# Kernel tuning notes

Hardware: AMD Instinct MI355X
Metric: run time of the kernel (lower is better)

Reference implementation:

```python
import jax, jax.numpy as jnp
import numpy as np

N = 2_097_152   # batched ODE RHS evaluation points
T = 10_000      # forcing time-series length (days)
H = 16          # MLP hidden width


def _step(x):
    # smooth Heaviside used throughout EXP-Hydro
    return (jnp.tanh(5.0 * x) + 1.0) * 0.5


def _mlp(x, W1, b1, W2, b2, W3, b3):
    h = jnp.tanh(x @ W1 + b1)
    h = jnp.tanh(h @ W2 + b2)
    return (h @ W3 + b3)[..., 0]


def setup_inputs() -> dict:
    key = jax.random.key(0)
    ks = jax.random.split(key, 16)
    ts = jnp.arange(T, dtype=jnp.float32)
    inp = {
        "t": jax.random.uniform(ks[0], (N,), jnp.float32) * (T - 1),
        "S_snow": jax.random.uniform(ks[1], (N,), jnp.float32) * 50.0,
        "S_water": jax.random.uniform(ks[2], (N,), jnp.float32) * 1000.0,
        "ts": ts,
        "precp_series": jax.random.uniform(ks[3], (T,), jnp.float32) * 20.0,
        "temp_series": jax.random.normal(ks[4], (T,), jnp.float32) * 10.0,
        "lday_series": 0.3 + 0.4 * jax.random.uniform(ks[5], (T,), jnp.float32),
        "etW1": jax.random.normal(ks[6], (3, H), jnp.float32) * (1.0 / np.sqrt(3)),
        "etb1": jnp.zeros((H,), jnp.float32),
        "etW2": jax.random.normal(ks[7], (H, H), jnp.float32) * (1.0 / np.sqrt(H)),
        "etb2": jnp.zeros((H,), jnp.float32),
        "etW3": jax.random.normal(ks[8], (H, 1), jnp.float32) * (1.0 / np.sqrt(H)),
        "etb3": jnp.zeros((1,), jnp.float32),
        "qW1": jax.random.normal(ks[9], (2, H), jnp.float32) * (1.0 / np.sqrt(2)),
        "qb1": jnp.zeros((H,), jnp.float32),
        "qW2": jax.random.normal(ks[10], (H, H), jnp.float32) * (1.0 / np.sqrt(H)),
        "qb2": jnp.zeros((H,), jnp.float32),
        "qW3": jax.random.normal(ks[11], (H, 1), jnp.float32) * (1.0 / np.sqrt(H)),
        "qb3": jnp.zeros((1,), jnp.float32),
        "Df": jnp.float32(2.674),
        "Tmax": jnp.float32(0.176),
        "Tmin": jnp.float32(-2.093),
    }
    return inp


def reference(t, S_snow, S_water, ts, precp_series, temp_series, lday_series,
              etW1, etb1, etW2, etb2, etW3, etb3,
              qW1, qb1, qW2, qb2, qW3, qb3,
              Df, Tmax, Tmin):
    # linear interpolation of forcings at query times t  -> [N]
    precp = jnp.interp(t, ts, precp_series)
    temp = jnp.interp(t, ts, temp_series)
    lday = jnp.interp(t, ts, lday_series)

    ET = _mlp(jnp.stack([S_snow, S_water, temp], axis=-1),
              etW1, etb1, etW2, etb2, etW3, etb3)          # [N]
    Q = _mlp(jnp.stack([S_water, precp], axis=-1),
             qW1, qb1, qW2, qb2, qW3, qb3)                 # [N]

    # bucket physics (M / Ps / Pr with smooth step)
    melt = _step(temp - Tmax) * _step(S_snow) * jnp.minimum(S_snow, Df * (temp - Tmax))
    Ps = _step(Tmin - temp) * precp   # snowfall
    Pr = _step(temp - Tmin) * precp   # rainfall
    sw = _step(S_water)

    dS_1 = Ps - melt
    dS_2 = Pr + melt - sw * lday * jnp.exp(ET) - sw * jnp.exp(Q)
    return (dS_1, dS_2)
```

## Files before the change

### kernel.cpp

```cpp
#include <hip/hip_runtime.h>
#include <math.h>

#define BLOCK 256
#define PPT   2

typedef _Float16 half2v __attribute__((ext_vector_type(2)));
typedef _Float16 half4v __attribute__((ext_vector_type(4)));
typedef float    float4v __attribute__((ext_vector_type(4)));

__device__ __forceinline__ half2v cvt_pk_h2(float a, float b) {
    return __builtin_bit_cast(half2v, __builtin_amdgcn_cvt_pkrtz(a, b));
}

__device__ __forceinline__ half4v mk_h4(unsigned w0, unsigned w1) {
    uint2 u; u.x = w0; u.y = w1;
    return __builtin_bit_cast(half4v, u);
}

#define H4(x) {(_Float16)(x), (_Float16)(x), (_Float16)(x), (_Float16)(x)}

__device__ __forceinline__ half4v tanh_pk4(half4v x) {
    const half4v c5 = H4(-3.71625e-05f);
    const half4v c4 = H4( 1.09648e-03f);
    const half4v c3 = H4(-1.288264e-02f);
    const half4v c2 = H4( 7.941906e-02f);
    const half4v c1 = H4(-3.0042735e-01f);
    const half4v c0 = H4( 9.9607644e-01f);
    const half4v hi = H4( 3.0f);
    const half4v lo = H4(-3.0f);
    half4v t = __builtin_elementwise_min(__builtin_elementwise_max(x, lo), hi);
    half4v s = t * t;
#if __has_builtin(__builtin_elementwise_fma)
    half4v p = __builtin_elementwise_fma(c5, s, c4);
    p = __builtin_elementwise_fma(p, s, c3);
    p = __builtin_elementwise_fma(p, s, c2);
    p = __builtin_elementwise_fma(p, s, c1);
    p = __builtin_elementwise_fma(p, s, c0);
#else
    half4v p = c5 * s + c4;
    p = p * s + c3;
    p = p * s + c2;
    p = p * s + c1;
    p = p * s + c0;
#endif
    return t * p;
}

__device__ __forceinline__ half4v pk4_from_f32(float a, float b, float c, float d) {
    half2v lo = cvt_pk_h2(a, b);
    half2v hi = cvt_pk_h2(c, d);
    return __builtin_shufflevector(lo, hi, 0, 1, 2, 3);
}

__device__ __forceinline__ half4v act4(float4v d) {
    return tanh_pk4(pk4_from_f32(d[0], d[1], d[2], d[3]));
}

#if __has_builtin(__builtin_amdgcn_permlane16_swap) && __has_builtin(__builtin_amdgcn_permlane32_swap)
#define SWAP16X(XV_) ({ auto _r = __builtin_amdgcn_permlane16_swap((XV_), (XV_), false, false); \
                        (unsigned)(_r[0] ^ _r[1] ^ (XV_)); })
#define SWAP32X(XV_) ({ auto _r = __builtin_amdgcn_permlane32_swap((XV_), (XV_), false, false); \
                        (unsigned)(_r[0] ^ _r[1] ^ (XV_)); })
#else
#define SWAP16X(XV_) ((unsigned)__shfl((int)(XV_), lane ^ 16, 64))
#define SWAP32X(XV_) ((unsigned)__shfl((int)(XV_), lane ^ 32, 64))
#endif

__global__ __launch_bounds__(BLOCK) void pack_forcings_kernel(
    const float* __restrict__ precp_s, const float* __restrict__ temp_s,
    const float* __restrict__ lday_s, float4* __restrict__ F, int T)
{
    int i = blockIdx.x * BLOCK + threadIdx.x;
    if (i < T) F[i] = make_float4(precp_s[i], temp_s[i], lday_s[i], 0.0f);
}

#define MFMA16(A, B, C) __builtin_amdgcn_mfma_f32_16x16x16f16((A), (B), (C), 0, 0, 0)

__global__ __launch_bounds__(BLOCK, 4) void exphydro_mfma_kernel(
    const float* __restrict__ t, const float* __restrict__ S_snow,
    const float* __restrict__ S_water,
    const float4* __restrict__ F,
    const float* __restrict__ etW1, const float* __restrict__ etb1,
    const float* __restrict__ etW2, const float* __restrict__ etb2,
    const float* __restrict__ etW3, const float* __restrict__ etb3,
    const float* __restrict__ qW1, const float* __restrict__ qb1,
    const float* __restrict__ qW2, const float* __restrict__ qb2,
    const float* __restrict__ qW3, const float* __restrict__ qb3,
    const float* __restrict__ pDf, const float* __restrict__ pTmax,
    const float* __restrict__ pTmin,
    float* __restrict__ out, int N, int T)
{
    const int lane = threadIdx.x & 63;
    const int hi   = lane >> 4;
    const int m    = lane & 15;
    const int wave = threadIdx.x >> 6;
    const int base = blockIdx.x * (BLOCK * PPT) + wave * (64 * PPT);

    half4v A1et, A1q, A2et, A2q, A3et, A3q;
    float4v C2et, C2q, C3et, C3q;
    #pragma unroll
    for (int j = 0; j < 4; j++) {
        int k = 4 * hi + j;
        float w1e = (k < 3) ? etW1[k * 16 + m] : ((k == 3) ? etb1[m] : 0.0f);
        float w1q = (k < 2) ? qW1 [k * 16 + m] : ((k == 2) ? qb1 [m] : 0.0f);
        A1et[j] = (_Float16)w1e;
        A1q [j] = (_Float16)w1q;
        A2et[j] = (_Float16)etW2[k * 16 + m];
        A2q [j] = (_Float16)qW2 [k * 16 + m];
        A3et[j] = (_Float16)etW3[k];
        A3q [j] = (_Float16)qW3 [k];
        C2et[j] = etb2[4 * hi + j];
        C2q [j] = qb2 [4 * hi + j];
        C3et[j] = etb3[0];
        C3q [j] = qb3 [0];
    }

    const float Df   = pDf[0];
    const float Tmax = pTmax[0];
    const float Tmin = pTmin[0];
    const float tmaxf = (float)(T - 1);
    const int   imax  = T - 2;

#define LOAD_POINT(U, Pv, SSv, SWv, TPv, PRv, LDv, I01v, I23v)                 \
    const int Pv = base + (U) * 64 + lane;                                     \
    float SSv, SWv, TPv, PRv, LDv; unsigned I01v, I23v;                        \
    {                                                                          \
        int pc = (Pv < N) ? Pv : (N - 1);                                      \
        float tv = t[pc];                                                      \
        SSv = S_snow[pc];                                                      \
        SWv = S_water[pc];                                                     \
        float tc = fminf(fmaxf(tv, 0.0f), tmaxf);                              \
        int i0 = (int)tc;                                                      \
        i0 = (i0 > imax) ? imax : i0;                                          \
        float fr = tc - (float)i0;                                             \
        float4 f0 = F[i0];                                                     \
        float4 f1 = F[i0 + 1];                                                 \
        PRv = fmaf(fr, f1.x - f0.x, f0.x);                                     \
        TPv = fmaf(fr, f1.y - f0.y, f0.y);                                     \
        LDv = fmaf(fr, f1.z - f0.z, f0.z);                                     \
        I01v = __builtin_bit_cast(unsigned, cvt_pk_h2(SSv, SWv));              \
        I23v = __builtin_bit_cast(unsigned, cvt_pk_h2(TPv, PRv));              \
    }

    LOAD_POINT(0, p0, ss0, sw0, tp0, pr0, ld0, i01_0, i23_0)
    LOAD_POINT(1, p1, ss1, sw1, tp1, pr1, ld1, i01_1, i23_1)

    const float4v zero4 = {0.0f, 0.0f, 0.0f, 0.0f};

#define MLP_SET(I01v, I23v, E0, E1, E2, E3, Q0, Q1, Q2, Q3)                    \
    float E0, E1, E2, E3, Q0, Q1, Q2, Q3;                                      \
    {                                                                          \
                              \
        unsigned j01_0 = I01v;                                                 \
        unsigned j23_0 = I23v;                                                 \
        unsigned j01_1 = SWAP16X(I01v);                                        \
        unsigned j23_1 = SWAP16X(I23v);                                        \
        unsigned j01_2 = SWAP32X(I01v);                                        \
        unsigned j23_2 = SWAP32X(I23v);                                        \
        unsigned j01_3 = SWAP16X(j01_2);                                       \
        unsigned j23_3 = SWAP16X(j23_2);                                       \
                                          \
        float4v d1e0 = MFMA16(A1et, mk_h4(j01_0, 0x3C000000u | (j23_0 & 0xFFFFu)), zero4); \
        float4v d1q0 = MFMA16(A1q,  mk_h4((j01_0 >> 16) | (j23_0 & 0xFFFF0000u), 0x3C00u), zero4); \
        float4v d1e1 = MFMA16(A1et, mk_h4(j01_1, 0x3C000000u | (j23_1 & 0xFFFFu)), zero4); \
        float4v d1q1 = MFMA16(A1q,  mk_h4((j01_1 >> 16) | (j23_1 & 0xFFFF0000u), 0x3C00u), zero4); \
        float4v d1e2 = MFMA16(A1et, mk_h4(j01_2, 0x3C000000u | (j23_2 & 0xFFFFu)), zero4); \
        float4v d1q2 = MFMA16(A1q,  mk_h4((j01_2 >> 16) | (j23_2 & 0xFFFF0000u), 0x3C00u), zero4); \
        float4v d1e3 = MFMA16(A1et, mk_h4(j01_3, 0x3C000000u | (j23_3 & 0xFFFFu)), zero4); \
        float4v d1q3 = MFMA16(A1q,  mk_h4((j01_3 >> 16) | (j23_3 & 0xFFFF0000u), 0x3C00u), zero4); \
                                       \
        half4v b2e0 = act4(d1e0);  half4v b2q0 = act4(d1q0);                   \
        half4v b2e1 = act4(d1e1);  half4v b2q1 = act4(d1q1);                   \
        half4v b2e2 = act4(d1e2);  half4v b2q2 = act4(d1q2);                   \
        half4v b2e3 = act4(d1e3);  half4v b2q3 = act4(d1q3);                   \
                                                          \
        float4v d2e0 = MFMA16(A2et, b2e0, C2et);  float4v d2q0 = MFMA16(A2q, b2q0, C2q); \
        float4v d2e1 = MFMA16(A2et, b2e1, C2et);  float4v d2q1 = MFMA16(A2q, b2q1, C2q); \
        float4v d2e2 = MFMA16(A2et, b2e2, C2et);  float4v d2q2 = MFMA16(A2q, b2q2, C2q); \
        float4v d2e3 = MFMA16(A2et, b2e3, C2et);  float4v d2q3 = MFMA16(A2q, b2q3, C2q); \
                                                       \
        half4v b3e0 = act4(d2e0);  half4v b3q0 = act4(d2q0);                   \
        half4v b3e1 = act4(d2e1);  half4v b3q1 = act4(d2q1);                   \
        half4v b3e2 = act4(d2e2);  half4v b3q2 = act4(d2q2);                   \
        half4v b3e3 = act4(d2e3);  half4v b3q3 = act4(d2q3);                   \
                                                          \
        float4v d3e0 = MFMA16(A3et, b3e0, C3et);  float4v d3q0 = MFMA16(A3q, b3q0, C3q); \
        float4v d3e1 = MFMA16(A3et, b3e1, C3et);  float4v d3q1 = MFMA16(A3q, b3q1, C3q); \
        float4v d3e2 = MFMA16(A3et, b3e2, C3et);  float4v d3q2 = MFMA16(A3q, b3q2, C3q); \
        float4v d3e3 = MFMA16(A3et, b3e3, C3et);  float4v d3q3 = MFMA16(A3q, b3q3, C3q); \
        E0 = d3e0[0]; E1 = d3e1[0]; E2 = d3e2[0]; E3 = d3e3[0];                \
        Q0 = d3q0[0]; Q1 = d3q1[0]; Q2 = d3q2[0]; Q3 = d3q3[0];                \
    }

    MLP_SET(i01_0, i23_0, et00, et01, et02, et03, q00, q01, q02, q03)
    MLP_SET(i01_1, i23_1, et10, et11, et12, et13, q10, q11, q12, q13)

#define FINISH_POINT(Pv, SSv, SWv, TPv, PRv, LDv, E0, E1, E2, E3, Q0, Q1, Q2, Q3) \
    {                                                                          \
        float e01s = (lane & 16) ? E1 : E0;                                    \
        float e23s = (lane & 16) ? E3 : E2;                                    \
        float ET   = (lane & 32) ? e23s : e01s;                                \
        float q01s = (lane & 16) ? Q1 : Q0;                                    \
        float q23s = (lane & 16) ? Q3 : Q2;                                    \
        float Q    = (lane & 32) ? q23s : q01s;                                \
        float dT = TPv - Tmax;                                                 \
        half4v sargs = pk4_from_f32(5.0f * dT, 5.0f * SSv,                     \
                                    5.0f * (Tmin - TPv), 5.0f * SWv);          \
        half4v th = tanh_pk4(sargs);                                           \
        float stepA  = fmaf(0.5f, (float)th[0], 0.5f);                         \
        float stepSn = fmaf(0.5f, (float)th[1], 0.5f);                         \
        float stepPs = fmaf(0.5f, (float)th[2], 0.5f);                         \
        float sw01   = fmaf(0.5f, (float)th[3], 0.5f);                         \
        float melt = stepA * stepSn * fminf(SSv, Df * dT);                     \
        float Ps   = stepPs * PRv;                                             \
        float Pr   = (1.0f - stepPs) * PRv;                                    \
        float dS1 = Ps - melt;                                                 \
        float dS2 = Pr + melt - sw01 * (LDv * __expf(ET) + __expf(Q));         \
        if (Pv < N) {                                                          \
            out[Pv]     = dS1;                                                 \
            out[N + Pv] = dS2;                                                 \
        }                                                                      \
    }

    FINISH_POINT(p0, ss0, sw0, tp0, pr0, ld0, et00, et01, et02, et03, q00, q01, q02, q03)
    FINISH_POINT(p1, ss1, sw1, tp1, pr1, ld1, et10, et11, et12, et13, q10, q11, q12, q13)
}

extern "C" void kernel_launch(void* const* d_in, const int* in_sizes, int n_in,
                              void* d_out, int out_size, void* d_ws, size_t ws_size,
                              hipStream_t stream) {
    const float* t        = (const float*)d_in[0];
    const float* S_snow   = (const float*)d_in[1];
    const float* S_water  = (const float*)d_in[2];
    const float* precp_s  = (const float*)d_in[4];
    const float* temp_s   = (const float*)d_in[5];
    const float* lday_s   = (const float*)d_in[6];
    const float* etW1     = (const float*)d_in[7];
    const float* etb1     = (const float*)d_in[8];
    const float* etW2     = (const float*)d_in[9];
    const float* etb2     = (const float*)d_in[10];
    const float* etW3     = (const float*)d_in[11];
    const float* etb3     = (const float*)d_in[12];
    const float* qW1      = (const float*)d_in[13];
    const float* qb1      = (const float*)d_in[14];
    const float* qW2      = (const float*)d_in[15];
    const float* qb2      = (const float*)d_in[16];
    const float* qW3      = (const float*)d_in[17];
    const float* qb3      = (const float*)d_in[18];
    const float* pDf      = (const float*)d_in[19];
    const float* pTmax    = (const float*)d_in[20];
    const float* pTmin    = (const float*)d_in[21];

    int N = in_sizes[0];
    int T = in_sizes[3];
    float* out = (float*)d_out;
    float4* F = (float4*)d_ws;

    pack_forcings_kernel<<<(T + BLOCK - 1) / BLOCK, BLOCK, 0, stream>>>(
        precp_s, temp_s, lday_s, F, T);

    int per_block = BLOCK * PPT;
    exphydro_mfma_kernel<<<(N + per_block - 1) / per_block, BLOCK, 0, stream>>>(
        t, S_snow, S_water, F,
        etW1, etb1, etW2, etb2, etW3, etb3,
        qW1, qb1, qW2, qb2, qW3, qb3,
        pDf, pTmax, pTmin, out, N, T);
}
```

Baseline: 41.80 us.

## Process four points per thread with all loads hoisted and per-point MLP scoping

Raises points per thread from 2 to 4, issuing every gather and load up front and then running the MLP and finish step one point at a time in separate scopes to bound register lifetimes. It also swaps the packed order of precipitation and temperature so the MFMA operand assembly uses a shift and alignbit instead of masks and ORs. The aim is more memory-level parallelism and fewer packing instructions, at the cost of higher register pressure and fewer blocks in the grid.

```diff
diff --git a/kernel.cpp b/kernel.cpp
--- a/kernel.cpp
+++ b/kernel.cpp
@@ -2,7 +2,7 @@
 #include <math.h>
 
 #define BLOCK 256
-#define PPT   2
+#define PPT   4
 
 typedef _Float16 half2v __attribute__((ext_vector_type(2)));
 typedef _Float16 half4v __attribute__((ext_vector_type(4)));
@@ -139,18 +139,19 @@
         TPv = fmaf(fr, f1.y - f0.y, f0.y);                                     \
         LDv = fmaf(fr, f1.z - f0.z, f0.z);                                     \
         I01v = __builtin_bit_cast(unsigned, cvt_pk_h2(SSv, SWv));              \
-        I23v = __builtin_bit_cast(unsigned, cvt_pk_h2(TPv, PRv));              \
+        I23v = __builtin_bit_cast(unsigned, cvt_pk_h2(PRv, TPv));              \
     }
 
     LOAD_POINT(0, p0, ss0, sw0, tp0, pr0, ld0, i01_0, i23_0)
     LOAD_POINT(1, p1, ss1, sw1, tp1, pr1, ld1, i01_1, i23_1)
+    LOAD_POINT(2, p2, ss2, sw2, tp2, pr2, ld2, i01_2, i23_2)
+    LOAD_POINT(3, p3, ss3, sw3, tp3, pr3, ld3, i01_3, i23_3)
 
     const float4v zero4 = {0.0f, 0.0f, 0.0f, 0.0f};
 
 #define MLP_SET(I01v, I23v, E0, E1, E2, E3, Q0, Q1, Q2, Q3)                    \
     float E0, E1, E2, E3, Q0, Q1, Q2, Q3;                                      \
     {                                                                          \
-                              \
         unsigned j01_0 = I01v;                                                 \
         unsigned j23_0 = I23v;                                                 \
         unsigned j01_1 = SWAP16X(I01v);                                        \
@@ -159,31 +160,26 @@
         unsigned j23_2 = SWAP32X(I23v);                                        \
         unsigned j01_3 = SWAP16X(j01_2);                                       \
         unsigned j23_3 = SWAP16X(j23_2);                                       \
-                                          \
-        float4v d1e0 = MFMA16(A1et, mk_h4(j01_0, 0x3C000000u | (j23_0 & 0xFFFFu)), zero4); \
-        float4v d1q0 = MFMA16(A1q,  mk_h4((j01_0 >> 16) | (j23_0 & 0xFFFF0000u), 0x3C00u), zero4); \
-        float4v d1e1 = MFMA16(A1et, mk_h4(j01_1, 0x3C000000u | (j23_1 & 0xFFFFu)), zero4); \
-        float4v d1q1 = MFMA16(A1q,  mk_h4((j01_1 >> 16) | (j23_1 & 0xFFFF0000u), 0x3C00u), zero4); \
-        float4v d1e2 = MFMA16(A1et, mk_h4(j01_2, 0x3C000000u | (j23_2 & 0xFFFFu)), zero4); \
-        float4v d1q2 = MFMA16(A1q,  mk_h4((j01_2 >> 16) | (j23_2 & 0xFFFF0000u), 0x3C00u), zero4); \
-        float4v d1e3 = MFMA16(A1et, mk_h4(j01_3, 0x3C000000u | (j23_3 & 0xFFFFu)), zero4); \
-        float4v d1q3 = MFMA16(A1q,  mk_h4((j01_3 >> 16) | (j23_3 & 0xFFFF0000u), 0x3C00u), zero4); \
-                                       \
+        float4v d1e0 = MFMA16(A1et, mk_h4(j01_0, 0x3C000000u | (j23_0 >> 16)), zero4); \
+        float4v d1q0 = MFMA16(A1q,  mk_h4(__builtin_amdgcn_alignbit(j23_0, j01_0, 16), 0x3C00u), zero4); \
+        float4v d1e1 = MFMA16(A1et, mk_h4(j01_1, 0x3C000000u | (j23_1 >> 16)), zero4); \
+        float4v d1q1 = MFMA16(A1q,  mk_h4(__builtin_amdgcn_alignbit(j23_1, j01_1, 16), 0x3C00u), zero4); \
+        float4v d1e2 = MFMA16(A1et, mk_h4(j01_2, 0x3C000000u | (j23_2 >> 16)), zero4); \
+        float4v d1q2 = MFMA16(A1q,  mk_h4(__builtin_amdgcn_alignbit(j23_2, j01_2, 16), 0x3C00u), zero4); \
+        float4v d1e3 = MFMA16(A1et, mk_h4(j01_3, 0x3C000000u | (j23_3 >> 16)), zero4); \
+        float4v d1q3 = MFMA16(A1q,  mk_h4(__builtin_amdgcn_alignbit(j23_3, j01_3, 16), 0x3C00u), zero4); \
         half4v b2e0 = act4(d1e0);  half4v b2q0 = act4(d1q0);                   \
         half4v b2e1 = act4(d1e1);  half4v b2q1 = act4(d1q1);                   \
         half4v b2e2 = act4(d1e2);  half4v b2q2 = act4(d1q2);                   \
         half4v b2e3 = act4(d1e3);  half4v b2q3 = act4(d1q3);                   \
-                                                          \
         float4v d2e0 = MFMA16(A2et, b2e0, C2et);  float4v d2q0 = MFMA16(A2q, b2q0, C2q); \
         float4v d2e1 = MFMA16(A2et, b2e1, C2et);  float4v d2q1 = MFMA16(A2q, b2q1, C2q); \
         float4v d2e2 = MFMA16(A2et, b2e2, C2et);  float4v d2q2 = MFMA16(A2q, b2q2, C2q); \
         float4v d2e3 = MFMA16(A2et, b2e3, C2et);  float4v d2q3 = MFMA16(A2q, b2q3, C2q); \
-                                                       \
         half4v b3e0 = act4(d2e0);  half4v b3q0 = act4(d2q0);                   \
         half4v b3e1 = act4(d2e1);  half4v b3q1 = act4(d2q1);                   \
         half4v b3e2 = act4(d2e2);  half4v b3q2 = act4(d2q2);                   \
         half4v b3e3 = act4(d2e3);  half4v b3q3 = act4(d2q3);                   \
-                                                          \
         float4v d3e0 = MFMA16(A3et, b3e0, C3et);  float4v d3q0 = MFMA16(A3q, b3q0, C3q); \
         float4v d3e1 = MFMA16(A3et, b3e1, C3et);  float4v d3q1 = MFMA16(A3q, b3q1, C3q); \
         float4v d3e2 = MFMA16(A3et, b3e2, C3et);  float4v d3q2 = MFMA16(A3q, b3q2, C3q); \
@@ -191,9 +187,6 @@
         E0 = d3e0[0]; E1 = d3e1[0]; E2 = d3e2[0]; E3 = d3e3[0];                \
         Q0 = d3q0[0]; Q1 = d3q1[0]; Q2 = d3q2[0]; Q3 = d3q3[0];                \
     }
-
-    MLP_SET(i01_0, i23_0, et00, et01, et02, et03, q00, q01, q02, q03)
-    MLP_SET(i01_1, i23_1, et10, et11, et12, et13, q10, q11, q12, q13)
 
 #define FINISH_POINT(Pv, SSv, SWv, TPv, PRv, LDv, E0, E1, E2, E3, Q0, Q1, Q2, Q3) \
     {                                                                          \
@@ -222,8 +215,22 @@
         }                                                                      \
     }
 
-    FINISH_POINT(p0, ss0, sw0, tp0, pr0, ld0, et00, et01, et02, et03, q00, q01, q02, q03)
-    FINISH_POINT(p1, ss1, sw1, tp1, pr1, ld1, et10, et11, et12, et13, q10, q11, q12, q13)
+    {
+        MLP_SET(i01_0, i23_0, et00, et01, et02, et03, q00, q01, q02, q03)
+        FINISH_POINT(p0, ss0, sw0, tp0, pr0, ld0, et00, et01, et02, et03, q00, q01, q02, q03)
+    }
+    {
+        MLP_SET(i01_1, i23_1, et10, et11, et12, et13, q10, q11, q12, q13)
+        FINISH_POINT(p1, ss1, sw1, tp1, pr1, ld1, et10, et11, et12, et13, q10, q11, q12, q13)
+    }
+    {
+        MLP_SET(i01_2, i23_2, et20, et21, et22, et23, q20, q21, q22, q23)
+        FINISH_POINT(p2, ss2, sw2, tp2, pr2, ld2, et20, et21, et22, et23, q20, q21, q22, q23)
+    }
+    {
+        MLP_SET(i01_3, i23_3, et30, et31, et32, et33, q30, q31, q32, q33)
+        FINISH_POINT(p3, ss3, sw3, tp3, pr3, ld3, et30, et31, et32, et33, q30, q31, q32, q33)
+    }
 }
 
 extern "C" void kernel_launch(void* const* d_in, const int* in_sizes, int n_in,
```

Measured after the change: 42.67 us. 2.1% more time.

## Convert to persistent grid-stride waves with software-pipelined prefetch of next tile

Applied to the files above, without the earlier changes.

Replaces the one-shot grid, where each wave handled two 64-point groups, with a fixed grid of 1024 blocks. Each wave loops over 128-point tiles in grid-stride fashion. Loads for the next tile (t, S_snow, S_water, then the forcing gathers) are issued before and after the current tile's MFMA MLP work, using double-buffered register sets to hide memory latency. This also amortises the per-wave weight setup across many tiles, at the cost of higher register pressure and possibly lower occupancy.

```diff
diff --git a/kernel.cpp b/kernel.cpp
--- a/kernel.cpp
+++ b/kernel.cpp
@@ -2,7 +2,7 @@
 #include <math.h>
 
 #define BLOCK 256
-#define PPT   2
+#define NBLK  1024
 
 typedef _Float16 half2v __attribute__((ext_vector_type(2)));
 typedef _Float16 half4v __attribute__((ext_vector_type(4)));
@@ -94,7 +94,9 @@
     const int hi   = lane >> 4;
     const int m    = lane & 15;
     const int wave = threadIdx.x >> 6;
-    const int base = blockIdx.x * (BLOCK * PPT) + wave * (64 * PPT);
+    const int wid    = blockIdx.x * (BLOCK / 64) + wave;
+    const int nwaves = gridDim.x * (BLOCK / 64);
+    const int ntiles = (N + 127) >> 7;
 
     half4v A1et, A1q, A2et, A2q, A3et, A3q;
     float4v C2et, C2q, C3et, C3q;
@@ -121,36 +123,54 @@
     const float tmaxf = (float)(T - 1);
     const int   imax  = T - 2;
 
-#define LOAD_POINT(U, Pv, SSv, SWv, TPv, PRv, LDv, I01v, I23v)                 \
-    const int Pv = base + (U) * 64 + lane;                                     \
-    float SSv, SWv, TPv, PRv, LDv; unsigned I01v, I23v;                        \
-    {                                                                          \
-        int pc = (Pv < N) ? Pv : (N - 1);                                      \
-        float tv = t[pc];                                                      \
-        SSv = S_snow[pc];                                                      \
-        SWv = S_water[pc];                                                     \
-        float tc = fminf(fmaxf(tv, 0.0f), tmaxf);                              \
-        int i0 = (int)tc;                                                      \
-        i0 = (i0 > imax) ? imax : i0;                                          \
-        float fr = tc - (float)i0;                                             \
-        float4 f0 = F[i0];                                                     \
-        float4 f1 = F[i0 + 1];                                                 \
-        PRv = fmaf(fr, f1.x - f0.x, f0.x);                                     \
-        TPv = fmaf(fr, f1.y - f0.y, f0.y);                                     \
-        LDv = fmaf(fr, f1.z - f0.z, f0.z);                                     \
-        I01v = __builtin_bit_cast(unsigned, cvt_pk_h2(SSv, SWv));              \
-        I23v = __builtin_bit_cast(unsigned, cvt_pk_h2(TPv, PRv));              \
-    }
-
-    LOAD_POINT(0, p0, ss0, sw0, tp0, pr0, ld0, i01_0, i23_0)
-    LOAD_POINT(1, p1, ss1, sw1, tp1, pr1, ld1, i01_1, i23_1)
+    if (wid >= ntiles) return;
+
+    float ntv0A, nss0A, nsw0A, ntv1A, nss1A, nsw1A;
+    float ntv0B, nss0B, nsw0B, ntv1B, nss1B, nsw1B;
+    int   pA0, pA1, pB0, pB1;
+    float ssA0, swA0, tpA0, prA0, ldA0, ssA1, swA1, tpA1, prA1, ldA1;
+    float ssB0, swB0, tpB0, prB0, ldB0, ssB1, swB1, tpB1, prB1, ldB1;
+    unsigned i01A0, i23A0, i01A1, i23A1;
+    unsigned i01B0, i23B0, i01B1, i23B1;
+
+#define LOADRAW(S, TILE) {                                                     \
+        int b_  = (TILE) * 128 + lane;                                         \
+        int c0_ = (b_ < N) ? b_ : (N - 1);                                     \
+        int b1_ = b_ + 64;                                                     \
+        int c1_ = (b1_ < N) ? b1_ : (N - 1);                                   \
+        ntv0##S = t[c0_]; nss0##S = S_snow[c0_]; nsw0##S = S_water[c0_];       \
+        ntv1##S = t[c1_]; nss1##S = S_snow[c1_]; nsw1##S = S_water[c1_];       \
+    }
+
+#define PREP1(TV, SSI, SWI, SSo, SWo, TPo, PRo, LDo, I01o, I23o) {             \
+        float tc_ = fminf(fmaxf((TV), 0.0f), tmaxf);                           \
+        int i0_ = (int)tc_;                                                    \
+        i0_ = (i0_ > imax) ? imax : i0_;                                       \
+        float fr_ = tc_ - (float)i0_;                                          \
+        float4 f0_ = F[i0_];                                                   \
+        float4 f1_ = F[i0_ + 1];                                               \
+        PRo = fmaf(fr_, f1_.x - f0_.x, f0_.x);                                 \
+        TPo = fmaf(fr_, f1_.y - f0_.y, f0_.y);                                 \
+        LDo = fmaf(fr_, f1_.z - f0_.z, f0_.z);                                 \
+        SSo = (SSI); SWo = (SWI);                                              \
+        I01o = __builtin_bit_cast(unsigned, cvt_pk_h2(SSo, SWo));              \
+        I23o = __builtin_bit_cast(unsigned, cvt_pk_h2(TPo, PRo));              \
+    }
+
+#define PREP(S, TILE) {                                                        \
+        p##S##0 = (TILE) * 128 + lane;                                         \
+        p##S##1 = p##S##0 + 64;                                                \
+        PREP1(ntv0##S, nss0##S, nsw0##S, ss##S##0, sw##S##0, tp##S##0,         \
+              pr##S##0, ld##S##0, i01##S##0, i23##S##0)                        \
+        PREP1(ntv1##S, nss1##S, nsw1##S, ss##S##1, sw##S##1, tp##S##1,         \
+              pr##S##1, ld##S##1, i01##S##1, i23##S##1)                        \
+    }
 
     const float4v zero4 = {0.0f, 0.0f, 0.0f, 0.0f};
 
 #define MLP_SET(I01v, I23v, E0, E1, E2, E3, Q0, Q1, Q2, Q3)                    \
     float E0, E1, E2, E3, Q0, Q1, Q2, Q3;                                      \
     {                                                                          \
-                              \
         unsigned j01_0 = I01v;                                                 \
         unsigned j23_0 = I23v;                                                 \
         unsigned j01_1 = SWAP16X(I01v);                                        \
@@ -159,7 +179,6 @@
         unsigned j23_2 = SWAP32X(I23v);                                        \
         unsigned j01_3 = SWAP16X(j01_2);                                       \
         unsigned j23_3 = SWAP16X(j23_2);                                       \
-                                          \
         float4v d1e0 = MFMA16(A1et, mk_h4(j01_0, 0x3C000000u | (j23_0 & 0xFFFFu)), zero4); \
         float4v d1q0 = MFMA16(A1q,  mk_h4((j01_0 >> 16) | (j23_0 & 0xFFFF0000u), 0x3C00u), zero4); \
         float4v d1e1 = MFMA16(A1et, mk_h4(j01_1, 0x3C000000u | (j23_1 & 0xFFFFu)), zero4); \
@@ -168,22 +187,18 @@
         float4v d1q2 = MFMA16(A1q,  mk_h4((j01_2 >> 16) | (j23_2 & 0xFFFF0000u), 0x3C00u), zero4); \
         float4v d1e3 = MFMA16(A1et, mk_h4(j01_3, 0x3C000000u | (j23_3 & 0xFFFFu)), zero4); \
         float4v d1q3 = MFMA16(A1q,  mk_h4((j01_3 >> 16) | (j23_3 & 0xFFFF0000u), 0x3C00u), zero4); \
-                                       \
         half4v b2e0 = act4(d1e0);  half4v b2q0 = act4(d1q0);                   \
         half4v b2e1 = act4(d1e1);  half4v b2q1 = act4(d1q1);                   \
         half4v b2e2 = act4(d1e2);  half4v b2q2 = act4(d1q2);                   \
         half4v b2e3 = act4(d1e3);  half4v b2q3 = act4(d1q3);                   \
-                                                          \
         float4v d2e0 = MFMA16(A2et, b2e0, C2et);  float4v d2q0 = MFMA16(A2q, b2q0, C2q); \
         float4v d2e1 = MFMA16(A2et, b2e1, C2et);  float4v d2q1 = MFMA16(A2q, b2q1, C2q); \
         float4v d2e2 = MFMA16(A2et, b2e2, C2et);  float4v d2q2 = MFMA16(A2q, b2q2, C2q); \
         float4v d2e3 = MFMA16(A2et, b2e3, C2et);  float4v d2q3 = MFMA16(A2q, b2q3, C2q); \
-                                                       \
         half4v b3e0 = act4(d2e0);  half4v b3q0 = act4(d2q0);                   \
         half4v b3e1 = act4(d2e1);  half4v b3q1 = act4(d2q1);                   \
         half4v b3e2 = act4(d2e2);  half4v b3q2 = act4(d2q2);                   \
         half4v b3e3 = act4(d2e3);  half4v b3q3 = act4(d2q3);                   \
-                                                          \
         float4v d3e0 = MFMA16(A3et, b3e0, C3et);  float4v d3q0 = MFMA16(A3q, b3q0, C3q); \
         float4v d3e1 = MFMA16(A3et, b3e1, C3et);  float4v d3q1 = MFMA16(A3q, b3q1, C3q); \
         float4v d3e2 = MFMA16(A3et, b3e2, C3et);  float4v d3q2 = MFMA16(A3q, b3q2, C3q); \
@@ -191,9 +206,6 @@
         E0 = d3e0[0]; E1 = d3e1[0]; E2 = d3e2[0]; E3 = d3e3[0];                \
         Q0 = d3q0[0]; Q1 = d3q1[0]; Q2 = d3q2[0]; Q3 = d3q3[0];                \
     }
-
-    MLP_SET(i01_0, i23_0, et00, et01, et02, et03, q00, q01, q02, q03)
-    MLP_SET(i01_1, i23_1, et10, et11, et12, et13, q10, q11, q12, q13)
 
 #define FINISH_POINT(Pv, SSv, SWv, TPv, PRv, LDv, E0, E1, E2, E3, Q0, Q1, Q2, Q3) \
     {                                                                          \
@@ -222,8 +234,40 @@
         }                                                                      \
     }
 
-    FINISH_POINT(p0, ss0, sw0, tp0, pr0, ld0, et00, et01, et02, et03, q00, q01, q02, q03)
-    FINISH_POINT(p1, ss1, sw1, tp1, pr1, ld1, et10, et11, et12, et13, q10, q11, q12, q13)
+#define HALF_ITER(CUR, NXT, NTC)                                               \
+    LOADRAW(NXT, NTC)                                                          \
+    MLP_SET(i01##CUR##0, i23##CUR##0, e0##CUR, e1##CUR, e2##CUR, e3##CUR,      \
+            g0##CUR, g1##CUR, g2##CUR, g3##CUR)                                \
+    MLP_SET(i01##CUR##1, i23##CUR##1, f0##CUR, f1##CUR, f2##CUR, f3##CUR,      \
+            h0##CUR, h1##CUR, h2##CUR, h3##CUR)                                \
+    PREP(NXT, NTC)                                                             \
+    FINISH_POINT(p##CUR##0, ss##CUR##0, sw##CUR##0, tp##CUR##0, pr##CUR##0,    \
+                 ld##CUR##0, e0##CUR, e1##CUR, e2##CUR, e3##CUR,               \
+                 g0##CUR, g1##CUR, g2##CUR, g3##CUR)                           \
+    FINISH_POINT(p##CUR##1, ss##CUR##1, sw##CUR##1, tp##CUR##1, pr##CUR##1,    \
+                 ld##CUR##1, f0##CUR, f1##CUR, f2##CUR, f3##CUR,               \
+                 h0##CUR, h1##CUR, h2##CUR, h3##CUR)
+
+    LOADRAW(A, wid)
+    PREP(A, wid)
+    int nxt = wid + nwaves;
+
+    for (;;) {
+        {
+            int  ntc  = (nxt < ntiles) ? nxt : wid;
+            bool last = (nxt >= ntiles);
+            HALF_ITER(A, B, ntc)
+            if (last) return;
+            nxt += nwaves;
+        }
+        {
+            int  ntc  = (nxt < ntiles) ? nxt : wid;
+            bool last = (nxt >= ntiles);
+            HALF_ITER(B, A, ntc)
+            if (last) return;
+            nxt += nwaves;
+        }
+    }
 }
 
 extern "C" void kernel_launch(void* const* d_in, const int* in_sizes, int n_in,
@@ -259,8 +303,7 @@
     pack_forcings_kernel<<<(T + BLOCK - 1) / BLOCK, BLOCK, 0, stream>>>(
         precp_s, temp_s, lday_s, F, T);
 
-    int per_block = BLOCK * PPT;
-    exphydro_mfma_kernel<<<(N + per_block - 1) / per_block, BLOCK, 0, stream>>>(
+    exphydro_mfma_kernel<<<NBLK, BLOCK, 0, stream>>>(
         t, S_snow, S_water, F,
         etW1, etb1, etW2, etb2, etW3, etb3,
         qW1, qb1, qW2, qb2, qW3, qb3,
```

After: 44.69 us. 6.9% more time.
